# Optimization experiments

Hardware: AMD Instinct MI355X
Metric: run time of the kernel (lower is better)

Reference implementation:

```python
import jax, jax.numpy as jnp
import numpy as np

OUT = 2048        # weight_size[0]
IN_BASE = 2048    # original input features
N_EMBED = 64      # replacements per iteration
IN_TOT = IN_BASE + 2 * N_EMBED  # 2176, weight_size[1]
NNZ_W = 400000
NNZ_B = 1024
BATCH = 8192


def setup_inputs() -> dict:
    key = jax.random.key(0)
    ks = jax.random.split(key, 10)
    return {
        "x": jax.random.normal(ks[0], (BATCH, IN_BASE), dtype=jnp.float32),
        "weight_vals": jax.random.normal(ks[1], (NNZ_W,), dtype=jnp.float32),
        "weight_rows": jax.random.randint(ks[2], (NNZ_W,), 0, OUT, dtype=jnp.int32),
        "weight_cols": jax.random.randint(ks[3], (NNZ_W,), 0, IN_TOT, dtype=jnp.int32),
        "bias_vals": jax.random.normal(ks[4], (NNZ_B,), dtype=jnp.float32),
        "bias_idx": jax.random.randint(ks[5], (NNZ_B,), 0, OUT, dtype=jnp.int32),
        "embed0_vals": jax.random.uniform(ks[6], (N_EMBED,), dtype=jnp.float32),
        "embed0_parents": jax.random.randint(ks[7], (N_EMBED,), 0, IN_BASE, dtype=jnp.int32),
        "embed1_vals": jax.random.uniform(ks[8], (N_EMBED,), dtype=jnp.float32),
        "embed1_parents": jax.random.randint(ks[9], (N_EMBED,), 0, IN_BASE + N_EMBED, dtype=jnp.int32),
    }


def reference(x, weight_vals, weight_rows, weight_cols, bias_vals, bias_idx,
              embed0_vals, embed0_parents, embed1_vals, embed1_parents):
    # EmbedLinear layers: each appends one new feature per stored row,
    # new_feat[:, c] = value[c] * x[:, parent[c]]  (single nnz per sparse row)
    x = jnp.concatenate([x, x[:, embed0_parents] * embed0_vals[None, :]], axis=1)  # [B, 2112]
    x = jnp.concatenate([x, x[:, embed1_parents] * embed1_vals[None, :]], axis=1)  # [B, 2176]
    # sparse weight -> dense via scatter-add (coalesce semantics sum duplicates)
    W = jnp.zeros((OUT, IN_TOT), dtype=weight_vals.dtype).at[weight_rows, weight_cols].add(weight_vals)
    b = jnp.zeros((OUT,), dtype=bias_vals.dtype).at[bias_idx].add(bias_vals)
    # (W @ x^T)^T + b  ==  x @ W^T + b
    return x @ W.T + b[None, :]
```

## Files before the change

### kernel.cpp

```cpp
#include <hip/hip_runtime.h>
#include <stdint.h>

#define OUT_F   2048
#define IN_BASE 2048
#define N_EMB   64
#define IN_TOT  2176
#define NNZ_W   400000
#define NNZ_B   1024
#define BATCH   8192

typedef __bf16 bf16x8 __attribute__((ext_vector_type(8)));
typedef __bf16 bf16x4 __attribute__((ext_vector_type(4)));
typedef float  floatx16 __attribute__((ext_vector_type(16)));

#define AS1 __attribute__((address_space(1)))
#define AS3 __attribute__((address_space(3)))

#define NSEG     391
#define SEG_NNZ  1024
#define CAP      24
#define NBIN     256
#define BIN_ELEMS (8 * IN_TOT)

#define NB_SCAT  NSEG
#define NB_BIAS  2
#define NB_BUILD BATCH

__global__ void __launch_bounds__(512) prep_kernel(
    const float* __restrict__ x,
    const float* __restrict__ e0v, const int* __restrict__ e0p,
    const float* __restrict__ e1v, const int* __restrict__ e1p,
    __bf16* __restrict__ xb,
    const float* __restrict__ wv, const int* __restrict__ wr,
    const int* __restrict__ wc,
    const float* __restrict__ bv, const int* __restrict__ bi,
    float* __restrict__ segv, unsigned short* __restrict__ segm,
    unsigned char* __restrict__ segc,
    float* __restrict__ bfp)
{
    const int tid = threadIdx.x;
    const int blk = blockIdx.x;

    if (blk < NB_SCAT) {
        __shared__ unsigned int hist[NBIN];
        if (tid < NBIN) hist[tid] = 0;
        __syncthreads();
#pragma unroll
        for (int r = 0; r < 2; r++) {
            const int i = blk * SEG_NNZ + r * 512 + tid;
            if (i < NNZ_W) {
                const int row = wr[i], col = wc[i];
                const int bin = row >> 3;
                const unsigned int rank = atomicAdd(&hist[bin], 1u);
                if (rank < CAP) {
                    const int p = (blk * NBIN + bin) * CAP + (int)rank;
                    segv[p] = wv[i];
                    segm[p] = (unsigned short)((row & 7) * IN_TOT + col);
                }
            }
        }
        __syncthreads();
        if (tid < NBIN)
            segc[blk * NBIN + tid] =
                (unsigned char)(hist[tid] < CAP ? hist[tid] : CAP);
    } else if (blk < NB_SCAT + NB_BIAS) {
        const int i = (blk - NB_SCAT) * 512 + tid;
        if (i < NNZ_B) unsafeAtomicAdd(bfp + bi[i], bv[i]);
    } else {
        const int b = blk - NB_SCAT - NB_BIAS;
        const float* xr = x + (size_t)b * IN_BASE;
        __bf16* xo = xb + (size_t)b * IN_TOT;

        {
            const float4 t = *(const float4*)(xr + tid * 4);
            bf16x4 o;
            o[0] = (__bf16)t.x; o[1] = (__bf16)t.y;
            o[2] = (__bf16)t.z; o[3] = (__bf16)t.w;
            *(bf16x4*)(xo + tid * 4) = o;
        }
        if (tid < 32) {
            const int g = 512 + tid;
            float v[4];
            if (g < 528) {
                const int j = (g - 512) * 4;
#pragma unroll
                for (int t = 0; t < 4; t++) v[t] = e0v[j + t] * xr[e0p[j + t]];
            } else {
                const int j = (g - 528) * 4;
#pragma unroll
                for (int t = 0; t < 4; t++) {
                    const int p = e1p[j + t];
                    const float base = (p < IN_BASE)
                        ? xr[p]
                        : e0v[p - IN_BASE] * xr[e0p[p - IN_BASE]];
                    v[t] = e1v[j + t] * base;
                }
            }
            bf16x4 o;
            o[0] = (__bf16)v[0]; o[1] = (__bf16)v[1];
            o[2] = (__bf16)v[2]; o[3] = (__bf16)v[3];
            *(bf16x4*)(xo + g * 4) = o;
        }
    }
}

__global__ void __launch_bounds__(512) accum_kernel(
    const float* __restrict__ segv, const unsigned short* __restrict__ segm,
    const unsigned char* __restrict__ segc,
    __bf16* __restrict__ Wb)
{
    __shared__ float Ws[BIN_ELEMS];
    const int tid = threadIdx.x;
    const int b   = blockIdx.x;

    for (int e = tid; e < BIN_ELEMS; e += 512) Ws[e] = 0.f;
    __syncthreads();

    for (int s = tid; s < NSEG; s += 512) {
        const int c    = segc[s * NBIN + b];
        const int base = (s * NBIN + b) * CAP;
        for (int j = 0; j < c; j++)
            atomicAdd(&Ws[segm[base + j]], segv[base + j]);
    }
    __syncthreads();

    __bf16* wo = Wb + (size_t)b * BIN_ELEMS;
    for (int e = tid; e < BIN_ELEMS / 4; e += 512) {
        bf16x4 o;
        o[0] = (__bf16)Ws[e * 4 + 0]; o[1] = (__bf16)Ws[e * 4 + 1];
        o[2] = (__bf16)Ws[e * 4 + 2]; o[3] = (__bf16)Ws[e * 4 + 3];
        *(bf16x4*)(wo + e * 4) = o;
    }
}

#define BM 256
#define BN 256
#define BK 64
#define NKT (IN_TOT / BK)
static_assert(NKT % 2 == 0, "loop consumes K-tiles in pairs");

#define CFENCE asm volatile("" ::: "memory")
#define BAR do { CFENCE; __builtin_amdgcn_s_barrier(); CFENCE; } while (0)
#define VMW(n) asm volatile("s_waitcnt vmcnt(" #n ")" ::: "memory")

#define STAGE(G, SBC, buf, tile, half) do {                                     \
    const __bf16* _s = (G) + (size_t)((half) * 128) * IN_TOT + (tile) * 64;     \
    char* _d = (SBC) + (buf) * 32768 + (half) * 16384 + tid * 16;               \
    __builtin_amdgcn_global_load_lds((AS1 void*)(uintptr_t)_s,                  \
                                     (AS3 void*)_d, 16, 0, 0);                  \
    __builtin_amdgcn_global_load_lds((AS1 void*)(uintptr_t)(_s + (size_t)64 * IN_TOT), \
                                     (AS3 void*)(_d + 8192), 16, 0, 0);         \
} while (0)

#define STAGE_T(buf, tile) do {                                                 \
    STAGE(Ag, sAc, buf, tile, 0);                                               \
    STAGE(Ag, sAc, buf, tile, 1);                                               \
    STAGE(Wg, sBc, buf, tile, 0);                                               \
    STAGE(Wg, sBc, buf, tile, 1);                                               \
} while (0)

#define RDS(as, bs, pA, pB, ks) do {                                            \
    const int kc = (ks) * 2 + khalf;                                            \
    _Pragma("unroll") for (int mq = 0; mq < 2; mq++)                            \
        _Pragma("unroll") for (int mi = 0; mi < 2; mi++) {                      \
            const int r = mq * 128 + wm * 64 + mi * 32 + l32;                   \
            as[mq * 2 + mi] = *(const bf16x8*)((pA) + r * 64 + ((kc ^ (r & 7)) * 8)); \
        }                                                                       \
    _Pragma("unroll") for (int nq = 0; nq < 2; nq++) {                          \
        const int rb = nq * 128 + wn * 32 + l32;                                \
        bs[nq] = *(const bf16x8*)((pB) + rb * 64 + ((kc ^ (rb & 7)) * 8));      \
    }                                                                           \
} while (0)

#define MMS(as, bs) do {                                                        \
    _Pragma("unroll") for (int mq = 0; mq < 2; mq++)                            \
        _Pragma("unroll") for (int mi = 0; mi < 2; mi++)                        \
            _Pragma("unroll") for (int nq = 0; nq < 2; nq++)                    \
                acc[mq][mi][nq] = __builtin_amdgcn_mfma_f32_32x32x16_bf16(      \
                    as[mq * 2 + mi], bs[nq], acc[mq][mi][nq], 0, 0, 0);         \
} while (0)

#define COMPUTE(buf) do {                                                       \
    const __bf16* _pA = sA + (buf) * 16384;                                     \
    const __bf16* _pB = sB + (buf) * 16384;                                     \
    RDS(aX, bX, _pA, _pB, 0);                                                   \
    RDS(aY, bY, _pA, _pB, 1);                                                   \
    MMS(aX, bX);                                                                \
    RDS(aX, bX, _pA, _pB, 2);                                                   \
    MMS(aY, bY);                                                                \
    RDS(aY, bY, _pA, _pB, 3);                                                   \
    MMS(aX, bX);                                                                \
    MMS(aY, bY);                                                                \
} while (0)

__global__ void __launch_bounds__(512, 2) gemm_kernel(
    const __bf16* __restrict__ A,
    const __bf16* __restrict__ W,
    const float*  __restrict__ bias,
    float* __restrict__ C)
{
    __shared__ __align__(16) __bf16 sA[2 * 256 * 64];
    __shared__ __align__(16) __bf16 sB[2 * 256 * 64];

    const int tid   = threadIdx.x;
    const int bm    = blockIdx.x;
    const int bn    = blockIdx.y;
    const int wave  = tid >> 6;
    const int lane  = tid & 63;
    const int wm    = wave >> 2;
    const int wn    = wave & 3;
    const int l32   = lane & 31;
    const int khalf = lane >> 5;

    floatx16 acc[2][2][2] = {};
    bf16x8 aX[4], bX[2];
    bf16x8 aY[4], bY[2];

    const int srow   = tid >> 3;
    const int kchunk = ((tid & 7) ^ ((tid >> 3) & 7)) * 8;
    const __bf16* Ag = A + (size_t)(bm * BM + srow) * IN_TOT + kchunk;
    const __bf16* Wg = W + (size_t)(bn * BN + srow) * IN_TOT + kchunk;
    char* sAc = (char*)sA;
    char* sBc = (char*)sB;

    STAGE_T(0, 0);
    VMW(0);
    BAR;

#pragma unroll 1
    for (int i = 0; i < NKT / 2 - 1; ++i) {
        STAGE_T(1, 2 * i + 1);
        COMPUTE(0);
        VMW(0);
        BAR;
        STAGE_T(0, 2 * i + 2);
        COMPUTE(1);
        VMW(0);
        BAR;
    }
    STAGE_T(1, NKT - 1);
    COMPUTE(0);
    VMW(0);
    BAR;
    COMPUTE(1);

#pragma unroll
    for (int m = 0; m < 2; m++)
#pragma unroll
    for (int mi = 0; mi < 2; mi++)
#pragma unroll
    for (int n = 0; n < 2; n++) {
        const int colg = bn * BN + n * 128 + wn * 32 + l32;
        const float bvv = bias[colg];
        const int rowb = bm * BM + m * 128 + wm * 64 + mi * 32 + 4 * khalf;
#pragma unroll
        for (int reg = 0; reg < 16; reg++) {
            const int rowg = rowb + (reg & 3) + 8 * (reg >> 2);
            C[(size_t)rowg * OUT_F + colg] = acc[m][mi][n][reg] + bvv;
        }
    }
}

extern "C" void kernel_launch(void* const* d_in, const int* in_sizes, int n_in,
                              void* d_out, int out_size, void* d_ws, size_t ws_size,
                              hipStream_t stream) {
    const float* x      = (const float*)d_in[0];
    const float* w_vals = (const float*)d_in[1];
    const int*   w_rows = (const int*)  d_in[2];
    const int*   w_cols = (const int*)  d_in[3];
    const float* b_vals = (const float*)d_in[4];
    const int*   b_idx  = (const int*)  d_in[5];
    const float* e0v    = (const float*)d_in[6];
    const int*   e0p    = (const int*)  d_in[7];
    const float* e1v    = (const float*)d_in[8];
    const int*   e1p    = (const int*)  d_in[9];
    float* out = (float*)d_out;

    char* ws = (char*)d_ws;
    const size_t W_BF16_BYTES = (size_t)OUT_F * IN_TOT * 2;
    const size_t B_F32_BYTES  = (size_t)OUT_F * 4;
    const size_t XB_BYTES     = (size_t)BATCH * IN_TOT * 2;
    const size_t SEGV_BYTES   = (size_t)NSEG * NBIN * CAP * 4;
    const size_t SEGM_BYTES   = (size_t)NSEG * NBIN * CAP * 2;
    __bf16*         Wb   = (__bf16*)ws;
    float*          bfp  = (float*)(ws + W_BF16_BYTES);
    __bf16*         xb   = (__bf16*)(ws + W_BF16_BYTES + B_F32_BYTES);
    float*          segv = (float*)(ws + W_BF16_BYTES + B_F32_BYTES + XB_BYTES);
    unsigned short* segm = (unsigned short*)((char*)segv + SEGV_BYTES);
    unsigned char*  segc = (unsigned char*)((char*)segm + SEGM_BYTES);

    hipMemsetAsync(bfp, 0, B_F32_BYTES, stream);

    prep_kernel<<<NB_SCAT + NB_BIAS + NB_BUILD, 512, 0, stream>>>(
        x, e0v, e0p, e1v, e1p, xb,
        w_vals, w_rows, w_cols, b_vals, b_idx,
        segv, segm, segc, bfp);

    accum_kernel<<<NBIN, 512, 0, stream>>>(segv, segm, segc, Wb);

    dim3 grid(BATCH / BM, OUT_F / BN);
    gemm_kernel<<<grid, 512, 0, stream>>>(xb, Wb, bfp, out);
}
```

Measured before the change: 217.6 us.

## Load A operand directly from global into registers, staging only W in LDS

The A (activation) tile is no longer staged through shared memory. Each wave loads its MFMA A fragments straight from global memory using per-row pointers, and only W is double-buffered in LDS. The K loop is rewritten to step one tile at a time with a dynamic buffer index. This halves LDS usage and drops the A staging traffic, but the four waves that share an A row each fetch it separately, the loads are strided by row, and their latency is no longer hidden by the staging pipeline.

Measured after the change: 313.1 us. 1.44x slower.

```diff
diff --git a/kernel.cpp b/kernel.cpp
--- a/kernel.cpp
+++ b/kernel.cpp
@@ -137,35 +137,29 @@
 #define BN 256
 #define BK 64
 #define NKT (IN_TOT / BK)
-static_assert(NKT % 2 == 0, "loop consumes K-tiles in pairs");
 
 #define CFENCE asm volatile("" ::: "memory")
 #define BAR do { CFENCE; __builtin_amdgcn_s_barrier(); CFENCE; } while (0)
 #define VMW(n) asm volatile("s_waitcnt vmcnt(" #n ")" ::: "memory")
 
-#define STAGE(G, SBC, buf, tile, half) do {                                     \
-    const __bf16* _s = (G) + (size_t)((half) * 128) * IN_TOT + (tile) * 64;     \
-    char* _d = (SBC) + (buf) * 32768 + (half) * 16384 + tid * 16;               \
+#define STAGE_B(buf, tile, half) do {                                           \
+    const __bf16* _s = Wg + (size_t)((half) * 128) * IN_TOT + (tile) * 64;      \
+    char* _d = sBc + (buf) * 32768 + (half) * 16384 + tid * 16;                 \
     __builtin_amdgcn_global_load_lds((AS1 void*)(uintptr_t)_s,                  \
                                      (AS3 void*)_d, 16, 0, 0);                  \
     __builtin_amdgcn_global_load_lds((AS1 void*)(uintptr_t)(_s + (size_t)64 * IN_TOT), \
                                      (AS3 void*)(_d + 8192), 16, 0, 0);         \
 } while (0)
 
-#define STAGE_T(buf, tile) do {                                                 \
-    STAGE(Ag, sAc, buf, tile, 0);                                               \
-    STAGE(Ag, sAc, buf, tile, 1);                                               \
-    STAGE(Wg, sBc, buf, tile, 0);                                               \
-    STAGE(Wg, sBc, buf, tile, 1);                                               \
-} while (0)
-
-#define RDS(as, bs, pA, pB, ks) do {                                            \
+#define RDA(as, t, ks) do {                                                     \
+    as[0] = *(const bf16x8*)(Ap0 + (t) * 64 + (ks) * 16);                       \
+    as[1] = *(const bf16x8*)(Ap1 + (t) * 64 + (ks) * 16);                       \
+    as[2] = *(const bf16x8*)(Ap2 + (t) * 64 + (ks) * 16);                       \
+    as[3] = *(const bf16x8*)(Ap3 + (t) * 64 + (ks) * 16);                       \
+} while (0)
+
+#define RDB(bs, pB, ks) do {                                                    \
     const int kc = (ks) * 2 + khalf;                                            \
-    _Pragma("unroll") for (int mq = 0; mq < 2; mq++)                            \
-        _Pragma("unroll") for (int mi = 0; mi < 2; mi++) {                      \
-            const int r = mq * 128 + wm * 64 + mi * 32 + l32;                   \
-            as[mq * 2 + mi] = *(const bf16x8*)((pA) + r * 64 + ((kc ^ (r & 7)) * 8)); \
-        }                                                                       \
     _Pragma("unroll") for (int nq = 0; nq < 2; nq++) {                          \
         const int rb = nq * 128 + wn * 32 + l32;                                \
         bs[nq] = *(const bf16x8*)((pB) + rb * 64 + ((kc ^ (rb & 7)) * 8));      \
@@ -180,15 +174,14 @@
                     as[mq * 2 + mi], bs[nq], acc[mq][mi][nq], 0, 0, 0);         \
 } while (0)
 
-#define COMPUTE(buf) do {                                                       \
-    const __bf16* _pA = sA + (buf) * 16384;                                     \
+#define COMPUTE(buf, t) do {                                                    \
     const __bf16* _pB = sB + (buf) * 16384;                                     \
-    RDS(aX, bX, _pA, _pB, 0);                                                   \
-    RDS(aY, bY, _pA, _pB, 1);                                                   \
+    RDA(aX, t, 0); RDB(bX, _pB, 0);                                             \
+    RDA(aY, t, 1); RDB(bY, _pB, 1);                                             \
     MMS(aX, bX);                                                                \
-    RDS(aX, bX, _pA, _pB, 2);                                                   \
+    RDA(aX, t, 2); RDB(bX, _pB, 2);                                             \
     MMS(aY, bY);                                                                \
-    RDS(aY, bY, _pA, _pB, 3);                                                   \
+    RDA(aY, t, 3); RDB(bY, _pB, 3);                                             \
     MMS(aX, bX);                                                                \
     MMS(aY, bY);                                                                \
 } while (0)
@@ -199,7 +192,6 @@
     const float*  __restrict__ bias,
     float* __restrict__ C)
 {
-    __shared__ __align__(16) __bf16 sA[2 * 256 * 64];
     __shared__ __align__(16) __bf16 sB[2 * 256 * 64];
 
     const int tid   = threadIdx.x;
@@ -216,33 +208,32 @@
     bf16x8 aX[4], bX[2];
     bf16x8 aY[4], bY[2];
 
+    const size_t rbase = (size_t)(bm * BM + wm * 64 + l32) * IN_TOT + khalf * 8;
+    const __bf16* Ap0 = A + rbase;
+    const __bf16* Ap1 = A + rbase + (size_t) 32 * IN_TOT;
+    const __bf16* Ap2 = A + rbase + (size_t)128 * IN_TOT;
+    const __bf16* Ap3 = A + rbase + (size_t)160 * IN_TOT;
+
     const int srow   = tid >> 3;
     const int kchunk = ((tid & 7) ^ ((tid >> 3) & 7)) * 8;
-    const __bf16* Ag = A + (size_t)(bm * BM + srow) * IN_TOT + kchunk;
     const __bf16* Wg = W + (size_t)(bn * BN + srow) * IN_TOT + kchunk;
-    char* sAc = (char*)sA;
     char* sBc = (char*)sB;
 
-    STAGE_T(0, 0);
+    STAGE_B(0, 0, 0);
+    STAGE_B(0, 0, 1);
     VMW(0);
     BAR;
 
 #pragma unroll 1
-    for (int i = 0; i < NKT / 2 - 1; ++i) {
-        STAGE_T(1, 2 * i + 1);
-        COMPUTE(0);
+    for (int t = 0; t < NKT - 1; ++t) {
+        const int cur = t & 1;
+        STAGE_B(cur ^ 1, t + 1, 0);
+        STAGE_B(cur ^ 1, t + 1, 1);
+        COMPUTE(cur, t);
         VMW(0);
         BAR;
-        STAGE_T(0, 2 * i + 2);
-        COMPUTE(1);
-        VMW(0);
-        BAR;
-    }
-    STAGE_T(1, NKT - 1);
-    COMPUTE(0);
-    VMW(0);
-    BAR;
-    COMPUTE(1);
+    }
+    COMPUTE((NKT - 1) & 1, NKT - 1);
 
 #pragma unroll
     for (int m = 0; m < 2; m++)
```
